# Kernel tuning notes

Measured on AMD Instinct MI355X. Metric: run time of the kernel, lower is better.

Reference implementation:

```python
import jax, jax.numpy as jnp
import numpy as np

N_HEADS = 16
ALIBI_BIAS_MAX = 8


def _alibi_bias(n_heads, seq_len):
    # MPT build_alibi_bias: bias[h, j] = -(seq_len-1-j) * slope_h, arranged [1,H,1,S]
    pos = jnp.arange(1 - seq_len, 1, dtype=jnp.float32).reshape(1, 1, 1, seq_len)
    m = jnp.arange(1, n_heads + 1, dtype=jnp.float32) * (ALIBI_BIAS_MAX / n_heads)
    slopes = (1.0 / jnp.exp2(m)).reshape(1, n_heads, 1, 1)
    return pos * slopes  # [1,H,1,S]


def setup_inputs() -> dict:
    key = jax.random.key(0)
    k1, k2, k3 = jax.random.split(key, 3)
    B, S, D = 1, 2048, 2048
    x = jax.random.normal(k1, (B, S, D), dtype=jnp.float32)
    # Wqkv: Linear(D, 3D, bias=False); out_proj: Linear(D, D, bias=False)
    w_qkv = jax.random.normal(k2, (3 * D, D), dtype=jnp.float32) * (1.0 / np.sqrt(D))
    w_out = jax.random.normal(k3, (D, D), dtype=jnp.float32) * (1.0 / np.sqrt(D))
    return {"x": x, "w_qkv": w_qkv, "w_out": w_out}


def reference(x, w_qkv, w_out):
    B, S, D = x.shape
    H = N_HEADS
    d = D // H
    qkv = x @ w_qkv.T                              # [B,S,3D]
    q, k, v = jnp.split(qkv, 3, axis=-1)
    q = q.reshape(B, S, H, d).transpose(0, 2, 1, 3)  # [B,H,S,d]
    k = k.reshape(B, S, H, d).transpose(0, 2, 1, 3)
    v = v.reshape(B, S, H, d).transpose(0, 2, 1, 3)
    scale = 1.0 / np.sqrt(d)
    scores = jnp.einsum('bhqd,bhkd->bhqk', q, k) * scale  # [B,H,S,S]
    scores = scores + _alibi_bias(H, S)
    min_val = jnp.finfo(scores.dtype).min
    causal = jnp.tril(jnp.ones((S, S), dtype=bool))
    scores = jnp.where(causal[None, None, :, :], scores, min_val)
    probs = jax.nn.softmax(scores.astype(jnp.float32), axis=-1).astype(q.dtype)
    out = jnp.einsum('bhqk,bhkd->bhqd', probs, v)  # [B,H,S,d]
    out = out.transpose(0, 2, 1, 3).reshape(B, S, D)
    return out @ w_out.T
```

## Files before the change

### kernel.cpp

```cpp
#include <hip/hip_runtime.h>

typedef __bf16 bf16;
typedef __bf16 bf16x8 __attribute__((ext_vector_type(8)));
typedef __bf16 bf16x4 __attribute__((ext_vector_type(4)));
typedef float f32x4 __attribute__((ext_vector_type(4)));

#if __has_builtin(__builtin_amdgcn_exp2f)
#define EXP2(x) __builtin_amdgcn_exp2f(x)
#else
#define EXP2(x) exp2f(x)
#endif

__device__ __forceinline__ void gload_lds16(const void* g, void* l) {
  __builtin_amdgcn_global_load_lds(
      (const __attribute__((address_space(1))) void*)g,
      (__attribute__((address_space(3))) void*)l, 16, 0, 0);
}

__global__ __launch_bounds__(256) void cast_all(const float* __restrict__ x,
                                                const float* __restrict__ wqkv,
                                                const float* __restrict__ wout,
                                                bf16* __restrict__ x_bf,
                                                bf16* __restrict__ wqkv_bf,
                                                bf16* __restrict__ wout_bf) {
  const int b = blockIdx.x;
  const float* src;
  bf16* dst;
  int i;
  if (b < 4096) {
    src = x; dst = x_bf; i = b * 1024 + threadIdx.x * 4;
  } else if (b < 16384) {
    src = wqkv; dst = wqkv_bf; i = (b - 4096) * 1024 + threadIdx.x * 4;
  } else {
    src = wout; dst = wout_bf; i = (b - 16384) * 1024 + threadIdx.x * 4;
  }
  float4 v = *(const float4*)(src + i);
  bf16x4 o = {(bf16)v.x, (bf16)v.y, (bf16)v.z, (bf16)v.w};
  *(bf16x4*)(dst + i) = o;
}

__global__ __launch_bounds__(256) void gemm1_qkv(const bf16* __restrict__ A,
                                                 const bf16* __restrict__ B,
                                                 bf16* __restrict__ qb,
                                                 bf16* __restrict__ kb,
                                                 bf16* __restrict__ vt) {
  constexpr int K = 2048;
  __shared__ bf16 As[128 * 32];
  __shared__ bf16 Bs[128 * 32];
  const int t = threadIdx.x;
  const int w = t >> 6, l = t & 63;
  const int lr = l & 15, lg = l >> 4;
  const int nwg = 768;
  int lin = blockIdx.y * 48 + blockIdx.x;
  lin = (lin & 7) * (nwg >> 3) + (lin >> 3);
  const int bn = lin % 48;
  const int bm = lin / 48;
  const int wr = w >> 1, wc = w & 1;

  f32x4 acc[4][4] = {};
  const int row0 = t >> 2;
  const int cc0 = (t & 3) * 8;

  for (int k0 = 0; k0 < K; k0 += 32) {
#pragma unroll
    for (int r = 0; r < 2; ++r) {
      const int row = r * 64 + row0;
      gload_lds16(A + (size_t)(bm * 128 + row) * K + k0 + cc0,
                  (char*)As + (r * 256 + w * 64) * 16);
      gload_lds16(B + (size_t)(bn * 128 + row) * K + k0 + cc0,
                  (char*)Bs + (r * 256 + w * 64) * 16);
    }
    __syncthreads();
    bf16x8 af[4], bfr[4];
#pragma unroll
    for (int i = 0; i < 4; ++i) {
      af[i] = *(const bf16x8*)((const char*)As + (wr * 64 + i * 16 + lr) * 64 + lg * 16);
      bfr[i] = *(const bf16x8*)((const char*)Bs + (wc * 64 + i * 16 + lr) * 64 + lg * 16);
    }
#pragma unroll
    for (int mi = 0; mi < 4; ++mi)
#pragma unroll
      for (int ni = 0; ni < 4; ++ni)
        acc[mi][ni] = __builtin_amdgcn_mfma_f32_16x16x32_bf16(af[mi], bfr[ni],
                                                              acc[mi][ni], 0, 0, 0);
    __syncthreads();
  }

  const int mb = bm * 128 + wr * 64 + lg * 4;
  const int nb = bn * 128 + wc * 64 + lr;
  if (bn * 128 < 4096) {
    bf16* dst = (bn * 128 < 2048) ? qb : kb;
#pragma unroll
    for (int mi = 0; mi < 4; ++mi) {
      const int mg = mb + mi * 16;
#pragma unroll
      for (int ni = 0; ni < 4; ++ni) {
        const int ng = (nb + ni * 16) & 2047;
#pragma unroll
        for (int rr = 0; rr < 4; ++rr)
          dst[(size_t)(mg + rr) * 2048 + ng] = (bf16)acc[mi][ni][rr];
      }
    }
  } else {
#pragma unroll
    for (int mi = 0; mi < 4; ++mi) {
      const int mg = mb + mi * 16;
#pragma unroll
      for (int ni = 0; ni < 4; ++ni) {
        const int dc = nb + ni * 16 - 4096;
        bf16x4 pk = {(bf16)acc[mi][ni][0], (bf16)acc[mi][ni][1],
                     (bf16)acc[mi][ni][2], (bf16)acc[mi][ni][3]};
        *(bf16x4*)(vt + (size_t)dc * 2048 + mg) = pk;
      }
    }
  }
}

__global__ __launch_bounds__(256) void gemm2_64x128(const bf16* __restrict__ A,
                                                    const bf16* __restrict__ B,
                                                    float* __restrict__ Cf) {
  constexpr int K = 2048, N = 2048;
  __shared__ bf16 As[64 * 32];
  __shared__ bf16 Bs[128 * 32];
  const int t = threadIdx.x;
  const int w = t >> 6, l = t & 63;
  const int lr = l & 15, lg = l >> 4;
  int lin = blockIdx.y * 16 + blockIdx.x;
  lin = (lin & 7) * 64 + (lin >> 3);
  const int bn = lin % 16;
  const int bm = lin / 16;

  f32x4 acc[4][2] = {};

  for (int k0 = 0; k0 < K; k0 += 32) {
    {
      const int row = t >> 2;
      gload_lds16(A + (size_t)(bm * 64 + row) * K + k0 + (t & 3) * 8,
                  (char*)As + (w * 64) * 16);
    }
#pragma unroll
    for (int r = 0; r < 2; ++r) {
      const int c = r * 256 + t;
      const int row = c >> 2;
      gload_lds16(B + (size_t)(bn * 128 + row) * K + k0 + (c & 3) * 8,
                  (char*)Bs + (r * 256 + w * 64) * 16);
    }
    __syncthreads();
    bf16x8 af[4], bfr[2];
#pragma unroll
    for (int i = 0; i < 4; ++i)
      af[i] = *(const bf16x8*)((const char*)As + (i * 16 + lr) * 64 + lg * 16);
#pragma unroll
    for (int i = 0; i < 2; ++i)
      bfr[i] = *(const bf16x8*)((const char*)Bs + (w * 32 + i * 16 + lr) * 64 + lg * 16);
#pragma unroll
    for (int mi = 0; mi < 4; ++mi)
#pragma unroll
      for (int ni = 0; ni < 2; ++ni)
        acc[mi][ni] = __builtin_amdgcn_mfma_f32_16x16x32_bf16(af[mi], bfr[ni],
                                                              acc[mi][ni], 0, 0, 0);
    __syncthreads();
  }

  const int mb = bm * 64 + lg * 4;
  const int nb = bn * 128 + w * 32 + lr;
#pragma unroll
  for (int mi = 0; mi < 4; ++mi) {
    const int mg = mb + mi * 16;
#pragma unroll
    for (int ni = 0; ni < 2; ++ni) {
      const int ng = nb + ni * 16;
#pragma unroll
      for (int rr = 0; rr < 4; ++rr)
        Cf[(size_t)(mg + rr) * N + ng] = acc[mi][ni][rr];
    }
  }
}

__global__ __launch_bounds__(256) void attn_kernel(const bf16* __restrict__ qb,
                                                   const bf16* __restrict__ kb,
                                                   const bf16* __restrict__ vt,
                                                   bf16* __restrict__ out,
                                                   bf16* __restrict__ pA,
                                                   bf16* __restrict__ pB,
                                                   float* __restrict__ ml) {
  constexpr int S = 2048, D = 2048;
  __shared__ bf16 Ks[2][64 * 128];
  __shared__ bf16 Vs[2][128 * 64];
  __shared__ bf16 Ps[4][16 * 64];
  const int t = threadIdx.x;
  const int w = t >> 6, l = t & 63;
  const int lr = l & 15, lg = l >> 4;
  const int b = blockIdx.x;

  int h, qt, piece, ns;
  if (b < 1024) {
    const int j = b >> 2;
    h = j & 15; qt = 16 + (j >> 4); piece = b & 3; ns = 4;
  } else if (b < 1280) {
    const int j = (b - 1024) >> 1;
    h = j & 15; qt = 8 + (j >> 4); piece = (b - 1024) & 1; ns = 2;
  } else {
    const int i = b - 1280;
    h = i & 15; qt = i >> 4; piece = 0; ns = 1;
  }
  const bool split = (ns > 1);
  const int q0 = qt * 64;
  const float slope2 = exp2f(-0.5f * (float)(h + 1)) * 1.4426950408889634f;
  const float scale2 = 0.08838834764831845f * 1.4426950408889634f;
  const int W = (int)(44.4f / slope2);
  const int s0 = (q0 > W) ? ((q0 - W) >> 6) : 0;
  const int len = qt + 1 - s0;
  const int start = s0 + (len * piece) / ns;
  const int end = s0 + (len * (piece + 1)) / ns;

  bf16x8 qf[4];
  {
    const bf16* qrow = qb + (size_t)(q0 + w * 16 + lr) * D + h * 128 + lg * 8;
#pragma unroll
    for (int kk = 0; kk < 4; ++kk) qf[kk] = *(const bf16x8*)(qrow + kk * 32);
  }

  f32x4 ob[8] = {};
  float mrow[4] = {-1e30f, -1e30f, -1e30f, -1e30f};
  float lrow[4] = {0.f, 0.f, 0.f, 0.f};

  auto stage = [&](int kv0, int bb) {
#pragma unroll
    for (int r = 0; r < 4; ++r) {
      {
        const int krow = r * 16 + (t >> 4);
        const int kcc = t & 15;
        gload_lds16(kb + (size_t)(kv0 + krow) * D + h * 128 + ((kcc ^ (krow & 7)) * 8),
                    (char*)Ks[bb] + (r * 256 + w * 64) * 16);
      }
      {
        const int vrow = r * 32 + (t >> 3);
        const int vcc = t & 7;
        gload_lds16(vt + (size_t)(h * 128 + vrow) * S + kv0 + ((vcc ^ (vrow & 7)) * 8),
                    (char*)Vs[bb] + (r * 256 + w * 64) * 16);
      }
    }
  };

  if (start < end) stage(start << 6, 0);
  int cur = 0;
  for (int tile = start; tile < end; ++tile) {
    __syncthreads();
    if (tile + 1 < end) stage((tile + 1) << 6, cur ^ 1);
    const int kv0 = tile << 6;

    f32x4 sc[4] = {};
    __builtin_amdgcn_s_setprio(1);
#pragma unroll
    for (int jb = 0; jb < 4; ++jb) {
      const int row = jb * 16 + lr;
#pragma unroll
      for (int kk = 0; kk < 4; ++kk) {
        const int byte = row * 256 + ((kk * 64 + lg * 16) ^ ((row & 7) << 4));
        bf16x8 kf = *(const bf16x8*)((const char*)Ks[cur] + byte);
        sc[jb] = __builtin_amdgcn_mfma_f32_16x16x32_bf16(qf[kk], kf, sc[jb], 0, 0, 0);
      }
    }
    __builtin_amdgcn_s_setprio(0);

    float bias[4];
#pragma unroll
    for (int jb = 0; jb < 4; ++jb)
      bias[jb] = slope2 * (float)(kv0 + jb * 16 + lr - (S - 1));
    const bool diag = (tile == qt);
    float xv[4][4], m2r[4];
#pragma unroll
    for (int rr = 0; rr < 4; ++rr) {
#pragma unroll
      for (int jb = 0; jb < 4; ++jb) {
        float v = fmaf(sc[jb][rr], scale2, bias[jb]);
        if (diag && (jb * 16 + lr > w * 16 + lg * 4 + rr)) v = -1e30f;
        xv[rr][jb] = v;
      }
      float m2 = fmaxf(fmaxf(xv[rr][0], xv[rr][1]), fmaxf(xv[rr][2], xv[rr][3]));
      m2 = fmaxf(m2, __shfl_xor(m2, 1));
      m2 = fmaxf(m2, __shfl_xor(m2, 2));
      m2 = fmaxf(m2, __shfl_xor(m2, 4));
      m2 = fmaxf(m2, __shfl_xor(m2, 8));
      m2r[rr] = m2;
    }
    float need = fmaxf(fmaxf(m2r[0] - mrow[0], m2r[1] - mrow[1]),
                       fmaxf(m2r[2] - mrow[2], m2r[3] - mrow[3]));
    if (!__all(need <= 8.0f)) {
#pragma unroll
      for (int rr = 0; rr < 4; ++rr) {
        const float mnew = fmaxf(mrow[rr], m2r[rr]);
        const float cf = EXP2(mrow[rr] - mnew);
        lrow[rr] *= cf;
        mrow[rr] = mnew;
#pragma unroll
        for (int db = 0; db < 8; ++db) ob[db][rr] *= cf;
      }
    }
    char* pbase = (char*)Ps[w];
#pragma unroll
    for (int rr = 0; rr < 4; ++rr) {
      const int prow = lg * 4 + rr;
      const int sw = (prow & 7) << 4;
      float ps = 0.f;
#pragma unroll
      for (int jb = 0; jb < 4; ++jb) {
        const float p = EXP2(xv[rr][jb] - mrow[rr]);
        *(bf16*)(pbase + ((prow * 128 + jb * 32 + lr * 2) ^ sw)) = (bf16)p;
        ps += p;
      }
      lrow[rr] += ps;
    }

    bf16x8 pf[2];
#pragma unroll
    for (int s = 0; s < 2; ++s)
      pf[s] = *(const bf16x8*)(pbase + ((lr * 128 + s * 64 + lg * 16) ^ ((lr & 7) << 4)));
    __builtin_amdgcn_s_setprio(1);
#pragma unroll
    for (int db = 0; db < 8; ++db) {
      const int vrow = db * 16 + lr;
#pragma unroll
      for (int s = 0; s < 2; ++s) {
        const int byte = vrow * 128 + ((s * 64 + lg * 16) ^ ((vrow & 7) << 4));
        bf16x8 vf = *(const bf16x8*)((const char*)Vs[cur] + byte);
        ob[db] = __builtin_amdgcn_mfma_f32_16x16x32_bf16(pf[s], vf, ob[db], 0, 0, 0);
      }
    }
    __builtin_amdgcn_s_setprio(0);
    cur ^= 1;
  }

  if (!split) {
#pragma unroll
    for (int rr = 0; rr < 4; ++rr) {
      float ls = lrow[rr];
      ls += __shfl_xor(ls, 1);
      ls += __shfl_xor(ls, 2);
      ls += __shfl_xor(ls, 4);
      ls += __shfl_xor(ls, 8);
      const float inv = 1.0f / ls;
      const int mg = q0 + w * 16 + lg * 4 + rr;
#pragma unroll
      for (int db = 0; db < 8; ++db)
        out[(size_t)mg * D + h * 128 + db * 16 + lr] = (bf16)(ob[db][rr] * inv);
    }
  } else {
    bf16* po = (b < 1024) ? pA + (size_t)b * 8192 : pB + (size_t)(b - 1024) * 8192;
#pragma unroll
    for (int rr = 0; rr < 4; ++rr) {
      float ls = lrow[rr];
      ls += __shfl_xor(ls, 1);
      ls += __shfl_xor(ls, 2);
      ls += __shfl_xor(ls, 4);
      ls += __shfl_xor(ls, 8);
      const int row = w * 16 + lg * 4 + rr;
#pragma unroll
      for (int db = 0; db < 8; ++db)
        po[row * 128 + db * 16 + lr] = (bf16)ob[db][rr];
      if (lr == 0) {
        ml[b * 128 + row] = mrow[rr];
        ml[b * 128 + 64 + row] = ls;
      }
    }
  }
}

__global__ __launch_bounds__(256) void attn_merge(const bf16* __restrict__ pA,
                                                  const bf16* __restrict__ pB,
                                                  const float* __restrict__ ml,
                                                  bf16* __restrict__ out) {
  const int j = blockIdx.x;
  const int t = threadIdx.x;
  int ns, c0, h, qt;
  if (j < 256) {
    ns = 4; c0 = 4 * j; h = j & 15; qt = 16 + (j >> 4);
  } else {
    const int j2 = j - 256;
    ns = 2; c0 = 1024 + 2 * j2; h = j2 & 15; qt = 8 + (j2 >> 4);
  }
  const int q0 = qt * 64;
  const int row = t >> 2;
  const int col0 = (t & 3) * 32;

  float m[4], lv[4];
  float M = -1e30f;
  for (int i = 0; i < ns; ++i) {
    m[i] = ml[(c0 + i) * 128 + row];
    lv[i] = ml[(c0 + i) * 128 + 64 + row];
    M = fmaxf(M, m[i]);
  }
  float wsum = 0.f, wgt[4];
  for (int i = 0; i < ns; ++i) {
    wgt[i] = EXP2(m[i] - M);
    wsum += wgt[i] * lv[i];
  }
  const float inv = 1.0f / wsum;

  float accv[32] = {};
  for (int i = 0; i < ns; ++i) {
    const int c = c0 + i;
    const bf16* po = (c < 1024) ? pA + (size_t)c * 8192 : pB + (size_t)(c - 1024) * 8192;
    const bf16* pr = po + row * 128 + col0;
    const float wi = wgt[i];
#pragma unroll
    for (int k = 0; k < 32; ++k) accv[k] += wi * (float)pr[k];
  }
  bf16* o = out + (size_t)(q0 + row) * 2048 + h * 128 + col0;
#pragma unroll
  for (int k = 0; k < 4; ++k) {
    bf16x8 o8;
#pragma unroll
    for (int e = 0; e < 8; ++e) o8[e] = (bf16)(accv[k * 8 + e] * inv);
    *(bf16x8*)(o + k * 8) = o8;
  }
}

extern "C" void kernel_launch(void* const* d_in, const int* in_sizes, int n_in,
                              void* d_out, int out_size, void* d_ws, size_t ws_size,
                              hipStream_t stream) {
  (void)in_sizes; (void)n_in; (void)out_size; (void)ws_size;
  const float* x = (const float*)d_in[0];
  const float* wqkv = (const float*)d_in[1];
  const float* wout = (const float*)d_in[2];
  float* out = (float*)d_out;

  bf16* x_bf = (bf16*)d_ws;
  bf16* wqkv_bf = x_bf + (size_t)2048 * 2048;
  bf16* wout_bf = wqkv_bf + (size_t)6144 * 2048;
  bf16* qb = wout_bf + (size_t)2048 * 2048;
  bf16* kb = qb + (size_t)2048 * 2048;
  bf16* vt = kb + (size_t)2048 * 2048;
  bf16* attn = wqkv_bf;
  bf16* pA = wqkv_bf + (size_t)2048 * 2048;
  bf16* pB = x_bf;
  float* ml = (float*)((char*)d_ws + (size_t)4 * 1024 * 1024);

  cast_all<<<20480, 256, 0, stream>>>(x, wqkv, wout, x_bf, wqkv_bf, wout_bf);
  gemm1_qkv<<<dim3(48, 16), 256, 0, stream>>>(x_bf, wqkv_bf, qb, kb, vt);
  attn_kernel<<<1408, 256, 0, stream>>>(qb, kb, vt, attn, pA, pB, ml);
  attn_merge<<<384, 256, 0, stream>>>(pA, pB, ml, attn);
  gemm2_64x128<<<dim3(16, 32), 256, 0, stream>>>(attn, wout_bf, out);
}
```

Before: 171.1 us.

## Load K and V fragments directly from global memory instead of LDS staging

Removes the double-buffered LDS staging of K and V tiles and the per-tile block barrier, so each wave reads its K and V MFMA operands straight from global memory (served by the L1/L2 caches). This drops LDS traffic, the async global-to-LDS copies and the __syncthreads, and frees shared memory for occupancy. In exchange, four waves now each fetch the same K/V data redundantly through the cache, and without explicit prefetch the global-load latency may be exposed right before the MFMAs.

```diff
diff --git a/kernel.cpp b/kernel.cpp
--- a/kernel.cpp
+++ b/kernel.cpp
@@ -185,8 +185,6 @@
                                                    bf16* __restrict__ pB,
                                                    float* __restrict__ ml) {
   constexpr int S = 2048, D = 2048;
-  __shared__ bf16 Ks[2][64 * 128];
-  __shared__ bf16 Vs[2][128 * 64];
   __shared__ bf16 Ps[4][16 * 64];
   const int t = threadIdx.x;
   const int w = t >> 6, l = t & 63;
@@ -225,40 +223,20 @@
   float mrow[4] = {-1e30f, -1e30f, -1e30f, -1e30f};
   float lrow[4] = {0.f, 0.f, 0.f, 0.f};
 
-  auto stage = [&](int kv0, int bb) {
-#pragma unroll
-    for (int r = 0; r < 4; ++r) {
-      {
-        const int krow = r * 16 + (t >> 4);
-        const int kcc = t & 15;
-        gload_lds16(kb + (size_t)(kv0 + krow) * D + h * 128 + ((kcc ^ (krow & 7)) * 8),
-                    (char*)Ks[bb] + (r * 256 + w * 64) * 16);
-      }
-      {
-        const int vrow = r * 32 + (t >> 3);
-        const int vcc = t & 7;
-        gload_lds16(vt + (size_t)(h * 128 + vrow) * S + kv0 + ((vcc ^ (vrow & 7)) * 8),
-                    (char*)Vs[bb] + (r * 256 + w * 64) * 16);
-      }
-    }
-  };
-
-  if (start < end) stage(start << 6, 0);
-  int cur = 0;
+  const bf16* kbase = kb + (size_t)lr * D + h * 128 + lg * 8;
+  const bf16* vbase = vt + (size_t)(h * 128 + lr) * S + lg * 8;
+
   for (int tile = start; tile < end; ++tile) {
-    __syncthreads();
-    if (tile + 1 < end) stage((tile + 1) << 6, cur ^ 1);
     const int kv0 = tile << 6;
 
     f32x4 sc[4] = {};
     __builtin_amdgcn_s_setprio(1);
 #pragma unroll
     for (int jb = 0; jb < 4; ++jb) {
-      const int row = jb * 16 + lr;
+      const bf16* kp = kbase + (size_t)(kv0 + jb * 16) * D;
 #pragma unroll
       for (int kk = 0; kk < 4; ++kk) {
-        const int byte = row * 256 + ((kk * 64 + lg * 16) ^ ((row & 7) << 4));
-        bf16x8 kf = *(const bf16x8*)((const char*)Ks[cur] + byte);
+        bf16x8 kf = *(const bf16x8*)(kp + kk * 32);
         sc[jb] = __builtin_amdgcn_mfma_f32_16x16x32_bf16(qf[kk], kf, sc[jb], 0, 0, 0);
       }
     }
@@ -317,19 +295,19 @@
 #pragma unroll
     for (int s = 0; s < 2; ++s)
       pf[s] = *(const bf16x8*)(pbase + ((lr * 128 + s * 64 + lg * 16) ^ ((lr & 7) << 4)));
+
+    const bf16* vp0 = vbase + kv0;
     __builtin_amdgcn_s_setprio(1);
 #pragma unroll
     for (int db = 0; db < 8; ++db) {
-      const int vrow = db * 16 + lr;
+      const bf16* vp = vp0 + (size_t)(db * 16) * S;
 #pragma unroll
       for (int s = 0; s < 2; ++s) {
-        const int byte = vrow * 128 + ((s * 64 + lg * 16) ^ ((vrow & 7) << 4));
-        bf16x8 vf = *(const bf16x8*)((const char*)Vs[cur] + byte);
+        bf16x8 vf = *(const bf16x8*)(vp + s * 32);
         ob[db] = __builtin_amdgcn_mfma_f32_16x16x32_bf16(pf[s], vf, ob[db], 0, 0, 0);
       }
     }
     __builtin_amdgcn_s_setprio(0);
-    cur ^= 1;
   }
 
   if (!split) {
```

Result: slower. 255.5 us (+49.4%).
